# Kernel optimization log

Measured on AMD Instinct MI355X. Metric: run time of the kernel, lower is better.

Reference implementation:

```python
import jax, jax.numpy as jnp
import numpy as np
from jax import lax

NPOINT = 1024
NSAMPLE = 64
RADIUS = 0.2
EPS = 1e-5  # BatchNorm eps


def farthest_point_sample(xyz, npoint):
    # xyz: [B, N, 3] -> idx [B, npoint]; deterministic init at point 0
    B, N, _ = xyz.shape

    def step(carry, _):
        dist, farthest = carry
        centroid = jnp.take_along_axis(xyz, farthest[:, None, None], axis=1)  # [B,1,3]
        d = jnp.sum((xyz - centroid) ** 2, axis=-1)  # [B,N]
        dist = jnp.minimum(dist, d)
        new_far = jnp.argmax(dist, axis=-1).astype(jnp.int32)
        return (dist, new_far), farthest

    init = (jnp.full((B, N), 1e10, xyz.dtype), jnp.zeros((B,), jnp.int32))
    _, idxs = lax.scan(step, init, None, length=npoint)
    return jnp.transpose(idxs)  # [B, npoint]


def square_distance(src, dst):
    # src [B,S,3], dst [B,N,3] -> [B,S,N]
    d = -2.0 * jnp.einsum('bsc,bnc->bsn', src, dst)
    d += jnp.sum(src ** 2, -1)[:, :, None]
    d += jnp.sum(dst ** 2, -1)[:, None, :]
    return d


def query_ball_point(radius, nsample, xyz, new_xyz):
    B, N, _ = xyz.shape
    sqr = square_distance(new_xyz, xyz)  # [B,S,N]
    gi = jnp.where(sqr > radius ** 2, N, jnp.arange(N, dtype=jnp.int32))
    gi = jnp.sort(gi, axis=-1)[:, :, :nsample]  # [B,S,K]
    first = gi[:, :, :1]
    gi = jnp.where(gi == N, first, gi)
    return gi


def mlp_bn_relu(x, W, g, b):
    # x [B,S,K,Cin], W [Cin,Cout]; 1x1 conv + training-mode BN + ReLU
    y = jnp.einsum('bskc,co->bsko', x, W)
    m = jnp.mean(y, axis=(0, 1, 2))
    v = jnp.var(y, axis=(0, 1, 2))
    y = (y - m) * lax.rsqrt(v + EPS) * g + b
    return jax.nn.relu(y)


def setup_inputs() -> dict:
    key = jax.random.key(0)
    ks = jax.random.split(key, 8)
    B, N, C = 8, 4096, 128
    xyz = jax.random.uniform(ks[0], (B, N, 3), dtype=jnp.float32)
    features = jax.random.normal(ks[1], (B, C, N), dtype=jnp.float32)
    c_in = C + 3  # use_xyz
    W1 = jax.random.normal(ks[2], (c_in, 128), dtype=jnp.float32) * 0.05
    W2 = jax.random.normal(ks[3], (128, 128), dtype=jnp.float32) * 0.05
    W3 = jax.random.normal(ks[4], (128, 256), dtype=jnp.float32) * 0.05
    return {
        'xyz': xyz, 'features': features,
        'W1': W1, 'g1': jnp.ones((128,)), 'b1': jnp.zeros((128,)),
        'W2': W2, 'g2': jnp.ones((128,)), 'b2': jnp.zeros((128,)),
        'W3': W3, 'g3': jnp.ones((256,)), 'b3': jnp.zeros((256,)),
    }


def reference(xyz, features, W1, g1, b1, W2, g2, b2, W3, g3, b3):
    fps_idx = farthest_point_sample(xyz, NPOINT)              # [B,S]
    new_xyz = jnp.take_along_axis(xyz, fps_idx[:, :, None], axis=1)  # [B,S,3]
    gi = query_ball_point(RADIUS, NSAMPLE, xyz, new_xyz)      # [B,S,K]
    gather = jax.vmap(lambda p, i: p[i])                      # per-batch gather
    grouped_xyz = gather(xyz, gi) - new_xyz[:, :, None, :]    # [B,S,K,3]
    grouped_feat = gather(jnp.transpose(features, (0, 2, 1)), gi)  # [B,S,K,C]
    x = jnp.concatenate([grouped_xyz, grouped_feat], axis=-1)  # [B,S,K,3+C]
    x = mlp_bn_relu(x, W1, g1, b1)
    x = mlp_bn_relu(x, W2, g2, b2)
    x = mlp_bn_relu(x, W3, g3, b3)
    new_features = jnp.transpose(jnp.max(x, axis=2), (0, 2, 1))  # [B,256,S]
    return new_xyz, new_features
```

## Files before the change

kernel.cpp:

```cpp
#include <hip/hip_runtime.h>

#define B_  8
#define N_  4096
#define S_  1024
#define K_  64
#define CF_ 128
#define M_  (B_*S_*K_)

typedef __attribute__((ext_vector_type(8))) short bshort8;
typedef __attribute__((ext_vector_type(4))) float f32x4;
typedef __attribute__((ext_vector_type(4))) int   i32x4;
typedef __attribute__((ext_vector_type(2))) float f32x2;

__device__ __forceinline__ unsigned short f2bf(float f){
  unsigned int u = __float_as_uint(f);
  u = u + 0x7FFFu + ((u >> 16) & 1u);
  return (unsigned short)(u >> 16);
}
__device__ __forceinline__ float bf2f(unsigned short h){
  return __uint_as_float(((unsigned int)h) << 16);
}

#define DPP_PAIR_STEP(CTRL)                                                     \
  {                                                                             \
    int _vi = __builtin_amdgcn_update_dpp(__float_as_int(best), __float_as_int(best), (CTRL), 0xF, 0xF, false); \
    int _ii = __builtin_amdgcn_update_dpp(bidx, bidx, (CTRL), 0xF, 0xF, false); \
    float _ov = __int_as_float(_vi);                                            \
    bool _tk = (_ov > best) || (_ov == best && _ii < bidx);                     \
    best = _tk ? _ov : best;                                                    \
    bidx = _tk ? _ii : bidx;                                                    \
  }

__global__ __launch_bounds__(256) void fps_kernel(const float* __restrict__ xyz,
                                                  float* __restrict__ nx_out,
                                                  float* __restrict__ nx_ws){
#pragma clang fp contract(off)
  __shared__ alignas(16) float sxyz[N_][4];
  __shared__ int   sidx[S_];
  __shared__ alignas(16) float redv[2][4];
  __shared__ alignas(16) int   redi[2][4];
  const int b = blockIdx.x, t = threadIdx.x;
  const int lane = t & 63, w = t >> 6;
  const float* xb = xyz + (size_t)b*N_*3;
  f32x2 px[8], py[8], pz[8], dist[8];
#pragma unroll
  for (int j=0;j<8;++j){
    int i0 = (2*j)*256 + t, i1 = (2*j+1)*256 + t;
    float x0=xb[i0*3+0], y0=xb[i0*3+1], z0=xb[i0*3+2];
    float x1=xb[i1*3+0], y1=xb[i1*3+1], z1=xb[i1*3+2];
    px[j] = (f32x2){x0,x1}; py[j] = (f32x2){y0,y1}; pz[j] = (f32x2){z0,z1};
    dist[j] = (f32x2){1e10f,1e10f};
    *(f32x4*)&sxyz[i0][0] = (f32x4){x0,y0,z0,0.f};
    *(f32x4*)&sxyz[i1][0] = (f32x4){x1,y1,z1,0.f};
  }
  __syncthreads();
  int farthest = 0;
  f32x4 cX = *(const f32x4*)&sxyz[0][0];
  float cx = cX[0], cy = cX[1], cz = cX[2];
  for (int it=0; it<S_; ++it){
    if (t==0) sidx[it] = farthest;
    f32x2 cx2 = (f32x2){cx,cx}, cy2 = (f32x2){cy,cy}, cz2 = (f32x2){cz,cz};
    float best = -1.0f; int bidx = 0;
#pragma unroll
    for (int j=0;j<8;++j){
      f32x2 dx = px[j] - cx2;
      f32x2 dy = py[j] - cy2;
      f32x2 dz = pz[j] - cz2;
      f32x2 d  = (dx*dx + dy*dy) + dz*dz;
      f32x2 nd;
      nd.x = fminf(dist[j].x, d.x);
      nd.y = fminf(dist[j].y, d.y);
      dist[j] = nd;
      bool tk0 = nd.x > best;
      best = tk0 ? nd.x : best;
      bidx = tk0 ? ((2*j)*256 + t) : bidx;
      bool tk1 = nd.y > best;
      best = tk1 ? nd.y : best;
      bidx = tk1 ? ((2*j+1)*256 + t) : bidx;
    }
    DPP_PAIR_STEP(0xB1);
    DPP_PAIR_STEP(0x4E);
    DPP_PAIR_STEP(0x124);
    DPP_PAIR_STEP(0x128);
    DPP_PAIR_STEP(0x142);
    DPP_PAIR_STEP(0x143);
    const int buf = it & 1;
    if (lane == 63){ redv[buf][w] = best; redi[buf][w] = bidx; }
    __syncthreads();
    f32x4 vv = *(const f32x4*)&redv[buf][0];
    i32x4 iv = *(const i32x4*)&redi[buf][0];
    f32x4 p0 = *(const f32x4*)&sxyz[iv[0]][0];
    f32x4 p1 = *(const f32x4*)&sxyz[iv[1]][0];
    f32x4 p2 = *(const f32x4*)&sxyz[iv[2]][0];
    f32x4 p3 = *(const f32x4*)&sxyz[iv[3]][0];
    bool t1 = (vv[1] > vv[0]) || (vv[1] == vv[0] && iv[1] < iv[0]);
    float va = t1 ? vv[1] : vv[0]; int ia = t1 ? iv[1] : iv[0];
    float ax = t1 ? p1[0] : p0[0], ay = t1 ? p1[1] : p0[1], az = t1 ? p1[2] : p0[2];
    bool t2 = (vv[3] > vv[2]) || (vv[3] == vv[2] && iv[3] < iv[2]);
    float vb = t2 ? vv[3] : vv[2]; int ib = t2 ? iv[3] : iv[2];
    float bx = t2 ? p3[0] : p2[0], by = t2 ? p3[1] : p2[1], bz = t2 ? p3[2] : p2[2];
    bool t3 = (vb > va) || (vb == va && ib < ia);
    farthest = t3 ? ib : ia;
    cx = t3 ? bx : ax; cy = t3 ? by : ay; cz = t3 ? bz : az;
  }
  __syncthreads();
  for (int i=t; i<S_; i+=256){
    int id = sidx[i];
    size_t base = (size_t)(b*S_+i)*3;
    float vx=sxyz[id][0], vy=sxyz[id][1], vz=sxyz[id][2];
    nx_out[base+0]=vx; nx_out[base+1]=vy; nx_out[base+2]=vz;
    nx_ws[base+0]=vx;  nx_ws[base+1]=vy;  nx_ws[base+2]=vz;
  }
}

__global__ __launch_bounds__(256) void qbp_kernel(const float* __restrict__ xyz,
                                                  const float* __restrict__ nx,
                                                  int* __restrict__ gi){
  const double R2 = 0.2*0.2;
  int gtid = blockIdx.x*256 + threadIdx.x;
  int wid = gtid >> 6, lane = gtid & 63;
  int b = wid >> 10, s = wid & 1023;
  const float* xb = xyz + (size_t)b*N_*3;
  const float* c  = nx + (size_t)(b*S_+s)*3;
  double cx=(double)c[0], cy=(double)c[1], cz=(double)c[2];
  double cc = cx*cx + cy*cy + cz*cz;
  int* g = gi + (size_t)(b*S_+s)*K_;
  int count = 0, first = -1;
  for (int ch=0; ch<64 && count<K_; ++ch){
    int i = ch*64 + lane;
    double x = (double)xb[i*3+0], y = (double)xb[i*3+1], z = (double)xb[i*3+2];
    double e  = cx*x + cy*y + cz*z;
    double pp = x*x + y*y + z*z;
    double d  = -2.0*e + cc + pp;
    bool keep = !(d > R2);
    unsigned long long bal = __ballot(keep);
    int pos = count + __builtin_popcountll(bal & ((1ull<<lane)-1ull));
    if (keep && pos < K_) g[pos] = i;
    if (first < 0 && bal) first = ch*64 + (int)__builtin_ctzll(bal);
    count += __builtin_popcountll(bal);
  }
  if (count < K_){
    int p = count + lane;
    if (p < K_) g[p] = first;
  }
}

__global__ __launch_bounds__(256) void transpose_kernel(const float* __restrict__ f,
                                                        unsigned short* __restrict__ ft){
  __shared__ float tile[32][33];
  int b = blockIdx.z, ct = blockIdx.y, nt = blockIdx.x;
  int tx = threadIdx.x & 31, ty = threadIdx.x >> 5;
#pragma unroll
  for (int r=0; r<32; r+=8)
    tile[ty+r][tx] = f[((size_t)(b*128 + ct*32 + ty + r))*4096 + nt*32 + tx];
  __syncthreads();
#pragma unroll
  for (int r=0; r<32; r+=8){
    int n = nt*32 + ty + r, cc = ct*32 + tx;
    ft[((size_t)b*4096 + n)*128 + cc] = f2bf(tile[tx][ty+r]);
  }
}

__global__ void wprep_kernel(const float* __restrict__ W1, const float* __restrict__ W2,
                             const float* __restrict__ W3,
                             unsigned short* __restrict__ Wt1, unsigned short* __restrict__ Wt2,
                             unsigned short* __restrict__ Wt3){
  int t = blockIdx.x*blockDim.x + threadIdx.x;
  int stride = gridDim.x*blockDim.x;
  for (int idx=t; idx<128*160; idx+=stride){
    int n = idx/160, k = idx-(idx/160)*160;
    float v = 0.f;
    if (k < 128) v = W1[(k+3)*128 + n];
    else if (k < 131) v = W1[(k-128)*128 + n];
    Wt1[idx] = f2bf(v);
  }
  for (int idx=t; idx<128*128; idx+=stride){
    int n = idx>>7, k = idx&127;
    Wt2[idx] = f2bf(W2[k*128+n]);
  }
  for (int idx=t; idx<256*128; idx+=stride){
    int n = idx>>7, k = idx&127;
    Wt3[idx] = f2bf(W3[k*256+n]);
  }
}

template<int PHASE>
__global__ __launch_bounds__(256,2) void mm_fused(
    const unsigned short* __restrict__ featT,
    const unsigned short* __restrict__ Wt1,
    const unsigned short* __restrict__ Wt2,
    const unsigned short* __restrict__ Wt3,
    const int* __restrict__ gi,
    const float* __restrict__ xyz,
    const float* __restrict__ nxyz,
    const float* __restrict__ ss1,
    const float* __restrict__ ss2,
    float* __restrict__ slots,
    float* __restrict__ minv,
    float* __restrict__ maxv)
{
  __shared__ alignas(16) unsigned short At[2][128*40];
  __shared__ alignas(16) unsigned short Bt[2][128*40];
  __shared__ alignas(16) unsigned short Y[(PHASE>=2)?(128*136):16];
  __shared__ int giL[128];

  const int t = threadIdx.x;
  const int mblk = blockIdx.x;
  const int b = mblk >> 9;
  const int lane = t&63, wave = t>>6;
  const int wm = wave>>1, wn = wave&1;
  const int lrow = lane&15, quad = lane>>4;
  const int slot = mblk & 63;

  if (t<128) giL[t] = gi[(size_t)mblk*128 + t];
  __syncthreads();

  f32x4 acc[4][4];
  const f32x4 z4 = {0.f,0.f,0.f,0.f};
#pragma unroll
  for (int i=0;i<4;++i)
#pragma unroll
    for (int j=0;j<4;++j) acc[i][j]=z4;

  {
    bshort8 aV[2], bV[2];
#pragma unroll
    for (int half=0; half<2; ++half){
      int sl = t + half*256; int r = sl>>2, p = sl&3;
      bV[half] = *(const bshort8*)(Wt1 + r*160 + p*8);
      int i = giL[r];
      aV[half] = *(const bshort8*)(featT + ((size_t)b*N_ + i)*CF_ + p*8);
    }
#pragma unroll
    for (int half=0; half<2; ++half){
      int sl = t + half*256; int r = sl>>2, p = sl&3;
      *(bshort8*)&At[0][r*40+p*8] = aV[half];
      *(bshort8*)&Bt[0][r*40+p*8] = bV[half];
    }
    for (int ch=0; ch<5; ++ch){
      const int cur = ch & 1;
      __syncthreads();
      bshort8 af[4], bfr[4];
#pragma unroll
      for (int mt=0; mt<4; ++mt) af[mt]  = *(const bshort8*)&At[cur][(wm*64+mt*16+lrow)*40 + quad*8];
#pragma unroll
      for (int nt=0; nt<4; ++nt) bfr[nt] = *(const bshort8*)&Bt[cur][(wn*64+nt*16+lrow)*40 + quad*8];
      if (ch < 4){
        const int nch = ch + 1;
#pragma unroll
        for (int half=0; half<2; ++half){
          int sl = t + half*256; int r = sl>>2, p = sl&3;
          bV[half] = *(const bshort8*)(Wt1 + r*160 + nch*32 + p*8);
          if (nch < 4){
            int i = giL[r];
            aV[half] = *(const bshort8*)(featT + ((size_t)b*N_ + i)*CF_ + nch*32 + p*8);
          } else {
            union { bshort8 v; unsigned short u[8]; } o;
#pragma unroll
            for (int e=0;e<8;++e) o.u[e]=0;
            if (p==0){
              int i = giL[r];
              int s = ((mblk*128 + r) >> 6) & 1023;
              const float* pp = xyz  + ((size_t)b*N_ + i)*3;
              const float* qq = nxyz + (size_t)(b*S_ + s)*3;
              o.u[0] = f2bf(__fsub_rn(pp[0],qq[0]));
              o.u[1] = f2bf(__fsub_rn(pp[1],qq[1]));
              o.u[2] = f2bf(__fsub_rn(pp[2],qq[2]));
            }
            aV[half] = o.v;
          }
        }
      }
#pragma unroll
      for (int mt=0; mt<4; ++mt)
#pragma unroll
        for (int nt=0; nt<4; ++nt)
          acc[mt][nt] = __builtin_amdgcn_mfma_f32_16x16x32_bf16(af[mt], bfr[nt], acc[mt][nt], 0,0,0);
      if (ch < 4){
        const int nxt = cur ^ 1;
#pragma unroll
        for (int half=0; half<2; ++half){
          int sl = t + half*256; int r = sl>>2, p = sl&3;
          *(bshort8*)&At[nxt][r*40+p*8] = aV[half];
          *(bshort8*)&Bt[nxt][r*40+p*8] = bV[half];
        }
      }
    }
  }

  if constexpr (PHASE==1){
#pragma unroll
    for (int nt=0; nt<4; ++nt){
      float s=0.f, s2=0.f;
#pragma unroll
      for (int mt=0; mt<4; ++mt)
#pragma unroll
        for (int r=0; r<4; ++r){ float v=acc[mt][nt][r]; s+=v; s2=fmaf(v,v,s2); }
      s  += __shfl_xor(s,16,64);  s  += __shfl_xor(s,32,64);
      s2 += __shfl_xor(s2,16,64); s2 += __shfl_xor(s2,32,64);
      if (lane<16){
        int c = wn*64+nt*16+lane;
        atomicAdd(&slots[(slot*128+c)*2+0], s);
        atomicAdd(&slots[(slot*128+c)*2+1], s2);
      }
    }
    return;
  }

  if constexpr (PHASE>=2){
#pragma unroll
    for (int nt=0; nt<4; ++nt){
      int c = wn*64+nt*16+lrow;
      float sc = ss1[c], sh = ss1[128+c];
#pragma unroll
      for (int mt=0; mt<4; ++mt)
#pragma unroll
        for (int r=0; r<4; ++r){
          int row = wm*64+mt*16+quad*4+r;
          Y[row*136 + c] = f2bf(fmaxf(fmaf(acc[mt][nt][r], sc, sh), 0.f));
        }
    }

#pragma unroll
    for (int i=0;i<4;++i)
#pragma unroll
      for (int j=0;j<4;++j) acc[i][j]=z4;
    {
      bshort8 bV[2];
#pragma unroll
      for (int half=0; half<2; ++half){
        int sl = t + half*256; int r = sl>>2, p = sl&3;
        bV[half] = *(const bshort8*)(Wt2 + r*128 + p*8);
      }
#pragma unroll
      for (int half=0; half<2; ++half){
        int sl = t + half*256; int r = sl>>2, p = sl&3;
        *(bshort8*)&Bt[1][r*40+p*8] = bV[half];
      }
      for (int ch=0; ch<4; ++ch){
        const int cur = (ch & 1) ^ 1;
        __syncthreads();
        bshort8 af[4], bfr[4];
#pragma unroll
        for (int mt=0; mt<4; ++mt) af[mt]  = *(const bshort8*)&Y[(wm*64+mt*16+lrow)*136 + ch*32 + quad*8];
#pragma unroll
        for (int nt=0; nt<4; ++nt) bfr[nt] = *(const bshort8*)&Bt[cur][(wn*64+nt*16+lrow)*40 + quad*8];
        if (ch < 3){
#pragma unroll
          for (int half=0; half<2; ++half){
            int sl = t + half*256; int r = sl>>2, p = sl&3;
            bV[half] = *(const bshort8*)(Wt2 + r*128 + (ch+1)*32 + p*8);
          }
        }
#pragma unroll
        for (int mt=0; mt<4; ++mt)
#pragma unroll
          for (int nt=0; nt<4; ++nt)
            acc[mt][nt] = __builtin_amdgcn_mfma_f32_16x16x32_bf16(af[mt], bfr[nt], acc[mt][nt], 0,0,0);
        if (ch < 3){
          const int nxt = cur ^ 1;
#pragma unroll
          for (int half=0; half<2; ++half){
            int sl = t + half*256; int r = sl>>2, p = sl&3;
            *(bshort8*)&Bt[nxt][r*40+p*8] = bV[half];
          }
        }
      }
    }
  }

  if constexpr (PHASE==2){
#pragma unroll
    for (int nt=0; nt<4; ++nt){
      float s=0.f, s2=0.f;
#pragma unroll
      for (int mt=0; mt<4; ++mt)
#pragma unroll
        for (int r=0; r<4; ++r){ float v=acc[mt][nt][r]; s+=v; s2=fmaf(v,v,s2); }
      s  += __shfl_xor(s,16,64);  s  += __shfl_xor(s,32,64);
      s2 += __shfl_xor(s2,16,64); s2 += __shfl_xor(s2,32,64);
      if (lane<16){
        int c = wn*64+nt*16+lane;
        atomicAdd(&slots[(slot*128+c)*2+0], s);
        atomicAdd(&slots[(slot*128+c)*2+1], s2);
      }
    }
    return;
  }

  if constexpr (PHASE==3){
    __syncthreads();
#pragma unroll
    for (int nt=0; nt<4; ++nt){
      int c = wn*64+nt*16+lrow;
      float sc = ss2[c], sh = ss2[128+c];
#pragma unroll
      for (int mt=0; mt<4; ++mt)
#pragma unroll
        for (int r=0; r<4; ++r){
          int row = wm*64+mt*16+quad*4+r;
          Y[row*136 + c] = f2bf(fmaxf(fmaf(acc[mt][nt][r], sc, sh), 0.f));
        }
    }

    for (int h=0; h<2; ++h){
#pragma unroll
      for (int i=0;i<4;++i)
#pragma unroll
        for (int j=0;j<4;++j) acc[i][j]=z4;
      bshort8 bV[2];
#pragma unroll
      for (int half=0; half<2; ++half){
        int sl = t + half*256; int r = sl>>2, p = sl&3;
        bV[half] = *(const bshort8*)(Wt3 + ((size_t)(h*128+r))*128 + p*8);
      }
#pragma unroll
      for (int half=0; half<2; ++half){
        int sl = t + half*256; int r = sl>>2, p = sl&3;
        *(bshort8*)&Bt[1][r*40+p*8] = bV[half];
      }
      for (int ch=0; ch<4; ++ch){
        const int cur = (ch & 1) ^ 1;
        __syncthreads();
        bshort8 af[4], bfr[4];
#pragma unroll
        for (int mt=0; mt<4; ++mt) af[mt]  = *(const bshort8*)&Y[(wm*64+mt*16+lrow)*136 + ch*32 + quad*8];
#pragma unroll
        for (int nt=0; nt<4; ++nt) bfr[nt] = *(const bshort8*)&Bt[cur][(wn*64+nt*16+lrow)*40 + quad*8];
        if (ch < 3){
#pragma unroll
          for (int half=0; half<2; ++half){
            int sl = t + half*256; int r = sl>>2, p = sl&3;
            bV[half] = *(const bshort8*)(Wt3 + ((size_t)(h*128+r))*128 + (ch+1)*32 + p*8);
          }
        }
#pragma unroll
        for (int mt=0; mt<4; ++mt)
#pragma unroll
          for (int nt=0; nt<4; ++nt)
            acc[mt][nt] = __builtin_amdgcn_mfma_f32_16x16x32_bf16(af[mt], bfr[nt], acc[mt][nt], 0,0,0);
        if (ch < 3){
          const int nxt = cur ^ 1;
#pragma unroll
          for (int half=0; half<2; ++half){
            int sl = t + half*256; int r = sl>>2, p = sl&3;
            *(bshort8*)&Bt[nxt][r*40+p*8] = bV[half];
          }
        }
      }
#pragma unroll
      for (int nt=0; nt<4; ++nt){
        float s=0.f, s2=0.f, mx=-3.0e38f, mn=3.0e38f;
#pragma unroll
        for (int mt=0; mt<4; ++mt)
#pragma unroll
          for (int r=0; r<4; ++r){
            float v=acc[mt][nt][r];
            s+=v; s2=fmaf(v,v,s2);
            mx=fmaxf(mx,v); mn=fminf(mn,v);
          }
        s  += __shfl_xor(s,16,64);  s  += __shfl_xor(s,32,64);
        s2 += __shfl_xor(s2,16,64); s2 += __shfl_xor(s2,32,64);
        mx = fmaxf(mx, __shfl_xor(mx,16,64)); mx = fmaxf(mx, __shfl_xor(mx,32,64));
        mn = fminf(mn, __shfl_xor(mn,16,64)); mn = fminf(mn, __shfl_xor(mn,32,64));
        if (lane<16){
          int c = h*128 + wn*64+nt*16+lane;
          atomicAdd(&slots[(slot*256+c)*2+0], s);
          atomicAdd(&slots[(slot*256+c)*2+1], s2);
          size_t sidx = (size_t)mblk*2 + wm;
          maxv[sidx*256 + c] = mx;
          minv[sidx*256 + c] = mn;
        }
      }
    }
  }
}

__global__ void stats_kernel(const float* __restrict__ slots, const float* __restrict__ g,
                             const float* __restrict__ beta, float* __restrict__ ssOut,
                             int C, float inv_cnt){
  int c = threadIdx.x;
  if (c >= C) return;
  float s=0.f, s2=0.f;
  for (int k=0;k<64;++k){
    s  += slots[(k*C + c)*2 + 0];
    s2 += slots[(k*C + c)*2 + 1];
  }
  float m = s * inv_cnt;
  float v = fmaxf(s2 * inv_cnt - m*m, 0.f);
  float sc = rsqrtf(v + 1e-5f) * g[c];
  ssOut[c] = sc;
  ssOut[C + c] = beta[c] - m*sc;
}

__global__ __launch_bounds__(256) void final_kernel(const float* __restrict__ minv,
                                                    const float* __restrict__ maxv,
                                                    const float* __restrict__ ss3,
                                                    float* __restrict__ out){
  __shared__ float tile[64][65];
  const int t = threadIdx.x;
  const int cb = blockIdx.x;
  const int sb = blockIdx.y;
  const int b  = blockIdx.z;
  const int w = t>>6, l = t&63;
  {
    int c = cb*64 + l;
    float sc = ss3[c], sh = ss3[256+c];
#pragma unroll
    for (int k=0;k<16;++k){
      int sl = k*4 + w;
      size_t mi = ((size_t)(b*1024 + sb*64 + sl))*256 + c;
      float v = (sc >= 0.f) ? maxv[mi] : minv[mi];
      tile[sl][l] = fmaxf(fmaf(v, sc, sh), 0.f);
    }
  }
  __syncthreads();
#pragma unroll
  for (int k=0;k<16;++k){
    int cl = k*4 + w;
    out[((size_t)(b*256 + cb*64 + cl))*1024 + sb*64 + l] = tile[l][cl];
  }
}

extern "C" void kernel_launch(void* const* d_in, const int* in_sizes, int n_in,
                              void* d_out, int out_size, void* d_ws, size_t ws_size,
                              hipStream_t stream){
  const float* xyz      = (const float*)d_in[0];
  const float* features = (const float*)d_in[1];
  const float* W1 = (const float*)d_in[2];
  const float* g1 = (const float*)d_in[3];
  const float* b1 = (const float*)d_in[4];
  const float* W2 = (const float*)d_in[5];
  const float* g2 = (const float*)d_in[6];
  const float* b2 = (const float*)d_in[7];
  const float* W3 = (const float*)d_in[8];
  const float* g3 = (const float*)d_in[9];
  const float* b3 = (const float*)d_in[10];
  float* out = (float*)d_out;

  char* ws = (char*)d_ws;
  size_t off = 0;
  auto alloc = [&](size_t bytes)->char*{
    char* p = ws + off;
    off = (off + bytes + 255) & ~(size_t)255;
    return p;
  };
  float* slots1 = (float*)alloc((size_t)64*128*2*4);
  float* slots2 = (float*)alloc((size_t)64*128*2*4);
  float* slots3 = (float*)alloc((size_t)64*256*2*4);
  float* ss1    = (float*)alloc(256*4);
  float* ss2    = (float*)alloc(256*4);
  float* ss3    = (float*)alloc(512*4);
  float* nxyz   = (float*)alloc((size_t)24576*4);
  int*   gi     = (int*)  alloc((size_t)M_*4);
  unsigned short* featT = (unsigned short*)alloc((size_t)B_*N_*CF_*2);
  unsigned short* Wt1   = (unsigned short*)alloc((size_t)128*160*2);
  unsigned short* Wt2   = (unsigned short*)alloc((size_t)128*128*2);
  unsigned short* Wt3   = (unsigned short*)alloc((size_t)256*128*2);
  float* minv = (float*)alloc((size_t)B_*S_*256*4);
  float* maxv = (float*)alloc((size_t)B_*S_*256*4);

  hipMemsetAsync(slots1, 0, (size_t)(64*128*2 + 64*128*2 + 64*256*2)*4, stream);

  transpose_kernel<<<dim3(128,4,8), 256, 0, stream>>>(features, featT);
  wprep_kernel<<<64, 256, 0, stream>>>(W1, W2, W3, Wt1, Wt2, Wt3);
  fps_kernel<<<8, 256, 0, stream>>>(xyz, out, nxyz);
  qbp_kernel<<<2048, 256, 0, stream>>>(xyz, nxyz, gi);

  const float inv_cnt = 1.0f / (float)M_;
  mm_fused<1><<<4096, 256, 0, stream>>>(featT, Wt1, Wt2, Wt3, gi, xyz, nxyz,
                                        nullptr, nullptr, slots1, nullptr, nullptr);
  stats_kernel<<<1, 128, 0, stream>>>(slots1, g1, b1, ss1, 128, inv_cnt);
  mm_fused<2><<<4096, 256, 0, stream>>>(featT, Wt1, Wt2, Wt3, gi, xyz, nxyz,
                                        ss1, nullptr, slots2, nullptr, nullptr);
  stats_kernel<<<1, 128, 0, stream>>>(slots2, g2, b2, ss2, 128, inv_cnt);
  mm_fused<3><<<4096, 256, 0, stream>>>(featT, Wt1, Wt2, Wt3, gi, xyz, nxyz,
                                        ss1, ss2, slots3, minv, maxv);
  stats_kernel<<<1, 256, 0, stream>>>(slots3, g3, b3, ss3, 256, inv_cnt);
  final_kernel<<<dim3(4,16,8), 256, 0, stream>>>(minv, maxv, ss3, out + 24576);
}
```

Before: 1.191 ms.

## Replace per-iteration FPS block barrier with tagged LDS spin-wait reduction

In the farthest-point-sampling loop, the per-iteration __syncthreads is replaced by lock-free handoff. Each wave's lane 63 writes a 16-byte record tagged with the iteration number at both ends into a double-buffered LDS slot. Every wave spins on volatile reads until all four records carry the current tag, which avoids a full workgroup barrier on each of the 1024 steps. Point coordinates move to structure-of-arrays LDS, and the centroid is loaded by index at the top of the next iteration instead of being selected alongside the reduction. The spin loop relies on 16-byte LDS writes being seen whole and adds LDS polling traffic while waves wait.

Measured after the change: 1.341 ms. +12.6%, slower.

```diff
diff --git a/kernel.cpp b/kernel.cpp
--- a/kernel.cpp
+++ b/kernel.cpp
@@ -35,10 +35,9 @@
                                                   float* __restrict__ nx_out,
                                                   float* __restrict__ nx_ws){
 #pragma clang fp contract(off)
-  __shared__ alignas(16) float sxyz[N_][4];
+  __shared__ float sx[N_], sy[N_], sz[N_];
   __shared__ int   sidx[S_];
-  __shared__ alignas(16) float redv[2][4];
-  __shared__ alignas(16) int   redi[2][4];
+  __shared__ alignas(16) int red[2][4][4];
   const int b = blockIdx.x, t = threadIdx.x;
   const int lane = t & 63, w = t >> 6;
   const float* xb = xyz + (size_t)b*N_*3;
@@ -50,15 +49,15 @@
     float x1=xb[i1*3+0], y1=xb[i1*3+1], z1=xb[i1*3+2];
     px[j] = (f32x2){x0,x1}; py[j] = (f32x2){y0,y1}; pz[j] = (f32x2){z0,z1};
     dist[j] = (f32x2){1e10f,1e10f};
-    *(f32x4*)&sxyz[i0][0] = (f32x4){x0,y0,z0,0.f};
-    *(f32x4*)&sxyz[i1][0] = (f32x4){x1,y1,z1,0.f};
-  }
+    sx[i0]=x0; sy[i0]=y0; sz[i0]=z0;
+    sx[i1]=x1; sy[i1]=y1; sz[i1]=z1;
+  }
+  if (t < 8) *(i32x4*)&red[t>>2][t&3][0] = (i32x4){-1,-1,-1,-1};
   __syncthreads();
   int farthest = 0;
-  f32x4 cX = *(const f32x4*)&sxyz[0][0];
-  float cx = cX[0], cy = cX[1], cz = cX[2];
   for (int it=0; it<S_; ++it){
     if (t==0) sidx[it] = farthest;
+    float cx = sx[farthest], cy = sy[farthest], cz = sz[farthest];
     f32x2 cx2 = (f32x2){cx,cx}, cy2 = (f32x2){cy,cy}, cz2 = (f32x2){cz,cz};
     float best = -1.0f; int bidx = 0;
 #pragma unroll
@@ -85,29 +84,31 @@
     DPP_PAIR_STEP(0x142);
     DPP_PAIR_STEP(0x143);
     const int buf = it & 1;
-    if (lane == 63){ redv[buf][w] = best; redi[buf][w] = bidx; }
-    __syncthreads();
-    f32x4 vv = *(const f32x4*)&redv[buf][0];
-    i32x4 iv = *(const i32x4*)&redi[buf][0];
-    f32x4 p0 = *(const f32x4*)&sxyz[iv[0]][0];
-    f32x4 p1 = *(const f32x4*)&sxyz[iv[1]][0];
-    f32x4 p2 = *(const f32x4*)&sxyz[iv[2]][0];
-    f32x4 p3 = *(const f32x4*)&sxyz[iv[3]][0];
-    bool t1 = (vv[1] > vv[0]) || (vv[1] == vv[0] && iv[1] < iv[0]);
-    float va = t1 ? vv[1] : vv[0]; int ia = t1 ? iv[1] : iv[0];
-    float ax = t1 ? p1[0] : p0[0], ay = t1 ? p1[1] : p0[1], az = t1 ? p1[2] : p0[2];
-    bool t2 = (vv[3] > vv[2]) || (vv[3] == vv[2] && iv[3] < iv[2]);
-    float vb = t2 ? vv[3] : vv[2]; int ib = t2 ? iv[3] : iv[2];
-    float bx = t2 ? p3[0] : p2[0], by = t2 ? p3[1] : p2[1], bz = t2 ? p3[2] : p2[2];
+    if (lane == 63){
+      *(i32x4*)&red[buf][w][0] = (i32x4){it, __float_as_int(best), bidx, it};
+    }
+    i32x4 s0, s1, s2, s3;
+    volatile i32x4* rp = (volatile i32x4*)&red[buf][0][0];
+    for (;;){
+      s0 = rp[0]; s1 = rp[1]; s2 = rp[2]; s3 = rp[3];
+      if (s0[0]==it && s0[3]==it && s1[0]==it && s1[3]==it &&
+          s2[0]==it && s2[3]==it && s3[0]==it && s3[3]==it) break;
+    }
+    float v0=__int_as_float(s0[1]), v1=__int_as_float(s1[1]);
+    float v2=__int_as_float(s2[1]), v3=__int_as_float(s3[1]);
+    int   i0=s0[2], i1=s1[2], i2=s2[2], i3=s3[2];
+    bool t1 = (v1 > v0) || (v1 == v0 && i1 < i0);
+    float va = t1 ? v1 : v0; int ia = t1 ? i1 : i0;
+    bool t2 = (v3 > v2) || (v3 == v2 && i3 < i2);
+    float vb = t2 ? v3 : v2; int ib = t2 ? i3 : i2;
     bool t3 = (vb > va) || (vb == va && ib < ia);
     farthest = t3 ? ib : ia;
-    cx = t3 ? bx : ax; cy = t3 ? by : ay; cz = t3 ? bz : az;
   }
   __syncthreads();
   for (int i=t; i<S_; i+=256){
     int id = sidx[i];
     size_t base = (size_t)(b*S_+i)*3;
-    float vx=sxyz[id][0], vy=sxyz[id][1], vz=sxyz[id][2];
+    float vx=sx[id], vy=sy[id], vz=sz[id];
     nx_out[base+0]=vx; nx_out[base+1]=vy; nx_out[base+2]=vz;
     nx_ws[base+0]=vx;  nx_ws[base+1]=vy;  nx_ws[base+2]=vz;
   }
```
